# Kernel optimization log

Hardware: AMD Instinct MI355X
Metric: run time of the kernel (lower is better)

The kernel has to match this reference:

```python
import jax, jax.numpy as jnp
import numpy as np

CH = (64, 128, 256, 512)
KV = 960
H = 4          # num_attention_heads; each head owns one channel quarter
EPS = 1e-5     # InstanceNorm2d default eps
B, N = 4, 4096

def _qsplit(x):
    # (B,n,c) -> (B,H,n,c//4): contiguous quarter-split along channels (torch .split)
    b, n, c = x.shape
    return x.reshape(b, n, H, c // H).transpose(0, 2, 1, 3)

def _kvsplit(emb_all):
    # quarter j of emb_all = concat over scales of quarter j of each scale's channel block
    b, n, _ = emb_all.shape
    parts, off = [], 0
    for c in CH:
        parts.append(emb_all[:, :, off:off + c].reshape(b, n, H, c // H))
        off += c
    return jnp.concatenate(parts, axis=-1).transpose(0, 2, 1, 3)  # (B,H,n,240)

def _inorm(s):
    # InstanceNorm2d(H), affine=False: normalize each (b,h) map over its (c,k) extent
    m = jnp.mean(s, axis=(2, 3), keepdims=True)
    v = jnp.var(s, axis=(2, 3), keepdims=True)
    return (s - m) * jax.lax.rsqrt(v + EPS)

def _attend(Q, K, V):
    # Q:(B,H,n,cq)  K,V:(B,H,n,240)  -> (B,n,H*cq)  (channel attention: contract over n)
    scores = jnp.einsum('bhnc,bhnk->bhck', Q, K) / np.float32(np.sqrt(KV))
    probs = jax.nn.softmax(_inorm(scores), axis=-1)
    ctx = jnp.einsum('bhck,bhnk->bnhc', probs, V)
    b, n = ctx.shape[:2]
    return ctx.reshape(b, n, -1)

def setup_inputs() -> dict:
    key = jax.random.key(0)
    ks = iter(jax.random.split(key, 48))
    d = {}
    for name, c in [('emb1', 64), ('emb2', 128), ('emb3', 256), ('emb4', 512)]:
        d[name] = jax.random.normal(next(ks), (B, N, c), jnp.float32)
        d[name.replace('emb', 'embd')] = jax.random.normal(next(ks), (B, N, c), jnp.float32)
    d['emb_all'] = jax.random.normal(next(ks), (B, N, KV), jnp.float32)
    d['emb_alld'] = jax.random.normal(next(ks), (B, N, KV), jnp.float32)
    sc = lambda f: float(1.0 / np.sqrt(f))
    for i, c in enumerate(CH):
        c4 = c // H
        d[f'wq{i+1}'] = jax.random.uniform(next(ks), (H, c4, c4), jnp.float32, -sc(c4), sc(c4))
        d[f'wqd{i+1}'] = jax.random.uniform(next(ks), (H, c4, c4), jnp.float32, -sc(c4), sc(c4))
        d[f'wout{i+1}'] = jax.random.uniform(next(ks), (c, c), jnp.float32, -sc(c), sc(c))
        d[f'woutd{i+1}'] = jax.random.uniform(next(ks), (c, c), jnp.float32, -sc(c), sc(c))
    k4 = KV // H
    for nm in ['wk', 'wv', 'wkd', 'wvd']:  # key/value weights are shared across quarters (module uses index [0])
        d[nm] = jax.random.uniform(next(ks), (k4, k4), jnp.float32, -sc(k4), sc(k4))
    return d

def reference(emb1, emb2, emb3, emb4, emb_all, embd1, embd2, embd3, embd4, emb_alld,
              wq1, wq2, wq3, wq4, wqd1, wqd2, wqd3, wqd4,
              wk, wv, wkd, wvd,
              wout1, wout2, wout3, wout4, woutd1, woutd2, woutd3, woutd4):
    Qs = [jnp.einsum('bhnc,hdc->bhnd', _qsplit(e), w) for e, w in
          zip((emb1, emb2, emb3, emb4), (wq1, wq2, wq3, wq4))]
    Qds = [jnp.einsum('bhnc,hdc->bhnd', _qsplit(e), w) for e, w in
           zip((embd1, embd2, embd3, embd4), (wqd1, wqd2, wqd3, wqd4))]
    kvq, kvqd = _kvsplit(emb_all), _kvsplit(emb_alld)
    K  = jnp.einsum('bhnc,dc->bhnd', kvq,  wk)
    V  = jnp.einsum('bhnc,dc->bhnd', kvq,  wv)
    Kd = jnp.einsum('bhnc,dc->bhnd', kvqd, wkd)
    Vd = jnp.einsum('bhnc,dc->bhnd', kvqd, wvd)
    outs = []
    # cross-modal: optical queries attend to DSM K/V and vice versa
    for Q, w in zip(Qs, (wout1, wout2, wout3, wout4)):
        outs.append(jnp.einsum('bnc,dc->bnd', _attend(Q, Kd, Vd), w))
    for Q, w in zip(Qds, (woutd1, woutd2, woutd3, woutd4)):
        outs.append(jnp.einsum('bnc,dc->bnd', _attend(Q, K, V), w))
    return jnp.concatenate(outs, axis=-1)  # (B, N, 2*960)
```

## Files before the change

kernel.cpp:

```cpp
#include <hip/hip_runtime.h>
#include <hip/hip_bf16.h>

typedef __bf16 bf16_t;
typedef __bf16 bf16x8 __attribute__((ext_vector_type(8)));
typedef float f32x4 __attribute__((ext_vector_type(4)));

static constexpr int B_ = 4, N_ = 4096, H_ = 4;
static constexpr int KS = 40;

__device__ __forceinline__ f32x4 mfma_bf16(bf16x8 a, bf16x8 b, f32x4 c) {
  return __builtin_amdgcn_mfma_f32_16x16x32_bf16(a, b, c, 0, 0, 0);
}

__device__ __forceinline__ void stpk4(bf16_t* d, float4 v) {
  bf16_t t[4] = {(bf16_t)v.x, (bf16_t)v.y, (bf16_t)v.z, (bf16_t)v.w};
  *(uint2*)d = *(const uint2*)t;
}
__device__ __forceinline__ void stz8(bf16_t* d) { *(uint2*)d = make_uint2(0u, 0u); }

__device__ __forceinline__ int kvg(int h, int c) {
  if (c < 16)  return h * 16 + c;
  if (c < 48)  return 64 + h * 32 + c - 16;
  if (c < 112) return 192 + h * 64 + c - 48;
  return 448 + h * 128 + c - 112;
}

__device__ __forceinline__ int qsc(int r) { return (r < 16) ? 0 : (r < 48) ? 1 : (r < 112) ? 2 : 3; }

__global__ __launch_bounds__(256) void k_prep_w(
    const float* __restrict__ wk, const float* __restrict__ wv,
    const float* __restrict__ wkd, const float* __restrict__ wvd,
    const float* __restrict__ wo00, const float* __restrict__ wo01,
    const float* __restrict__ wo02, const float* __restrict__ wo03,
    const float* __restrict__ wo10, const float* __restrict__ wo11,
    const float* __restrict__ wo12, const float* __restrict__ wo13,
    bf16_t* __restrict__ Wkvb, bf16_t* __restrict__ Wob) {
  const float* wkv[4] = {wk, wv, wkd, wvd};
  const float* wo[2][4] = {{wo00, wo01, wo02, wo03}, {wo10, wo11, wo12, wo13}};
  const int soff_f4[5] = {0, 1024, 5120, 21504, 87040};
  for (int i = blockIdx.x * 256 + threadIdx.x; i < 231680; i += gridDim.x * 256) {
    if (i < 57600) {
      int t = i / 14400, r = i - t * 14400;
      float4 v = *(const float4*)(wkv[t] + r * 4);
      stpk4(Wkvb + (size_t)t * 57600 + r * 4, v);
    } else {
      int j = i - 57600;
      int mod = j / 87040, jr = j - mod * 87040;
      int s = (jr < 1024) ? 0 : (jr < 5120) ? 1 : (jr < 21504) ? 2 : 3;
      float4 v = *(const float4*)(wo[mod][s] + (jr - soff_f4[s]) * 4);
      stpk4(Wob + (size_t)mod * 348160 + jr * 4, v);
    }
  }
}

__global__ __launch_bounds__(256) void k_kvsplit(
    const float* __restrict__ eA, const float* __restrict__ eB,
    bf16_t* __restrict__ G) {
  const int TOT = 2 * 16 * 4096 * 30;
  for (int i = blockIdx.x * 256 + threadIdx.x; i < TOT; i += gridDim.x * 256) {
    int t = i / 30;
    int cg = i - t * 30;
    int mod = t >> 16;
    int row = t & 65535;
    int bh = row >> 12, n = row & 4095;
    int b = bh >> 2, h = bh & 3;
    int col = kvg(h, cg * 8);
    const float* src = (mod ? eB : eA) + ((size_t)b * N_ + n) * 960 + col;
    float4 v0 = *(const float4*)src;
    float4 v1 = *(const float4*)(src + 4);
    bf16_t o[8] = {(bf16_t)v0.x, (bf16_t)v0.y, (bf16_t)v0.z, (bf16_t)v0.w,
                   (bf16_t)v1.x, (bf16_t)v1.y, (bf16_t)v1.z, (bf16_t)v1.w};
    *(uint4*)(G + (size_t)t * 240 + cg * 8) = *(const uint4*)o;
  }
}

template <int C4>
__global__ __launch_bounds__(256) void k_proj_q(
    const float* __restrict__ e0, const float* __restrict__ w0, bf16_t* __restrict__ o0,
    const float* __restrict__ e1, const float* __restrict__ w1, bf16_t* __restrict__ o1) {
  constexpr int KP = (C4 < 32) ? 32 : C4;
  constexpr int NF = C4 / 16;
  const float* emb = blockIdx.z ? e1 : e0;
  const float* wq = blockIdx.z ? w1 : w0;
  bf16_t* qout = blockIdx.z ? o1 : o0;
  const int h = blockIdx.y;
  const int m0 = blockIdx.x * 128;
  const int b = m0 >> 12, n0 = m0 & 4095;
  const int tid = threadIdx.x, lane = tid & 63, wid = tid >> 6;
  const int l15 = lane & 15, q = lane >> 4;
  __shared__ bf16_t sA[128 * KS];
  __shared__ bf16_t sB[C4 * KS];
  const f32x4 fz = {0.f, 0.f, 0.f, 0.f};
  f32x4 acc[2][NF];
  for (int i = 0; i < 2; i++) for (int f = 0; f < NF; f++) acc[i][f] = fz;
  const float* srow = emb + ((size_t)b * N_ + n0) * (H_ * C4) + h * C4;
  const float* wb = wq + h * C4 * C4;
  for (int k0 = 0; k0 < KP; k0 += 32) {
    __syncthreads();
    for (int idx = tid; idx < 1024; idx += 256) {
      int r = idx >> 3, cg = idx & 7, c = k0 + cg * 4;
      if (c < C4) stpk4(&sA[r * KS + cg * 4], *(const float4*)(srow + (size_t)r * (H_ * C4) + c));
      else stz8(&sA[r * KS + cg * 4]);
    }
    for (int idx = tid; idx < C4 * 8; idx += 256) {
      int dd = idx >> 3, cg = idx & 7, c = k0 + cg * 4;
      if (c < C4) stpk4(&sB[dd * KS + cg * 4], *(const float4*)(wb + dd * C4 + c));
      else stz8(&sB[dd * KS + cg * 4]);
    }
    __syncthreads();
    const bf16_t* ap = &sA[(wid * 32 + l15) * KS + q * 8];
    bf16x8 a0 = *(const bf16x8*)ap;
    bf16x8 a1 = *(const bf16x8*)(ap + 16 * KS);
    for (int f = 0; f < NF; f++) {
      bf16x8 bb = *(const bf16x8*)&sB[(16 * f + l15) * KS + q * 8];
      acc[0][f] = mfma_bf16(a0, bb, acc[0][f]);
      acc[1][f] = mfma_bf16(a1, bb, acc[1][f]);
    }
  }
  bf16_t* qbh = qout + (size_t)(b * H_ + h) * C4 * 4096;
  for (int i = 0; i < 2; i++)
    for (int f = 0; f < NF; f++) {
      bf16_t pk[4];
      for (int r = 0; r < 4; r++) pk[r] = (bf16_t)acc[i][f][r];
      *(uint2*)(qbh + (size_t)(16 * f + l15) * 4096 + n0 + wid * 32 + 16 * i + q * 4) =
          *(const uint2*)pk;
    }
}

__global__ __launch_bounds__(512) void k_proj_kv(
    const bf16_t* __restrict__ G, const bf16_t* __restrict__ Wkvb,
    bf16_t* __restrict__ Kt0, bf16_t* __restrict__ V0,
    bf16_t* __restrict__ Kt1, bf16_t* __restrict__ V1) {
  const int mod = blockIdx.y;
  const bf16_t* src = G + (size_t)mod * ((size_t)B_ * H_ * N_ * 240);
  const bf16_t* wK = Wkvb + (size_t)(2 * mod) * 57600;
  const bf16_t* wV = Wkvb + (size_t)(2 * mod + 1) * 57600;
  bf16_t* Kt = mod ? Kt1 : Kt0;
  bf16_t* V = mod ? V1 : V0;
  const int m0 = blockIdx.x * 128;
  const int bh = m0 >> 12, n0 = m0 & 4095;
  const int tid = threadIdx.x, lane = tid & 63, wid = tid >> 6;
  const int l15 = lane & 15, q = lane >> 4;
  __shared__ bf16_t sA[128 * KS];
  __shared__ bf16_t sB[2][240 * KS];
  const f32x4 fz = {0.f, 0.f, 0.f, 0.f};
  f32x4 accK[15], accV[15];
  for (int f = 0; f < 15; f++) { accK[f] = fz; accV[f] = fz; }
  const bf16_t* arow = src + (size_t)m0 * 240;
  const uint4 z4 = make_uint4(0u, 0u, 0u, 0u);

  const int ar = tid >> 2, ag = tid & 3;
  int bm[4], bd[4], bg[4];
#pragma unroll
  for (int j = 0; j < 4; j++) {
    int idx = tid + 512 * j;
    bm[j] = idx >= 960;
    int jj = idx - (bm[j] ? 960 : 0);
    bd[j] = jj >> 2; bg[j] = jj & 3;
  }
  uint4 ra, rb0, rb1, rb2, rb3;

#define KV_LOAD(K0)                                                                    \
  {                                                                                    \
    int c = (K0) + ag * 8;                                                             \
    ra = (c < 240) ? *(const uint4*)(arow + (size_t)ar * 240 + c) : z4;                \
    int c0_ = (K0) + bg[0] * 8;                                                        \
    rb0 = (c0_ < 240) ? *(const uint4*)((bm[0] ? wV : wK) + bd[0] * 240 + c0_) : z4;   \
    int c1_ = (K0) + bg[1] * 8;                                                        \
    rb1 = (c1_ < 240) ? *(const uint4*)((bm[1] ? wV : wK) + bd[1] * 240 + c1_) : z4;   \
    int c2_ = (K0) + bg[2] * 8;                                                        \
    rb2 = (c2_ < 240) ? *(const uint4*)((bm[2] ? wV : wK) + bd[2] * 240 + c2_) : z4;   \
    if (tid < 384) {                                                                   \
      int c3_ = (K0) + bg[3] * 8;                                                      \
      rb3 = (c3_ < 240) ? *(const uint4*)((bm[3] ? wV : wK) + bd[3] * 240 + c3_) : z4; \
    }                                                                                  \
  }
#define KV_WRITE()                                                                     \
  {                                                                                    \
    *(uint4*)&sA[ar * KS + ag * 8] = ra;                                               \
    *(uint4*)&sB[bm[0]][bd[0] * KS + bg[0] * 8] = rb0;                                 \
    *(uint4*)&sB[bm[1]][bd[1] * KS + bg[1] * 8] = rb1;                                 \
    *(uint4*)&sB[bm[2]][bd[2] * KS + bg[2] * 8] = rb2;                                 \
    if (tid < 384) *(uint4*)&sB[bm[3]][bd[3] * KS + bg[3] * 8] = rb3;                  \
  }

  KV_LOAD(0);
  KV_WRITE();
  for (int t = 0; t < 8; t++) {
    if (t < 7) KV_LOAD((t + 1) * 32);
    __syncthreads();
    bf16x8 a = *(const bf16x8*)&sA[(wid * 16 + l15) * KS + q * 8];
#pragma unroll
    for (int f = 0; f < 15; f++) {
      bf16x8 bk = *(const bf16x8*)&sB[0][(16 * f + l15) * KS + q * 8];
      bf16x8 bv = *(const bf16x8*)&sB[1][(16 * f + l15) * KS + q * 8];
      accK[f] = mfma_bf16(a, bk, accK[f]);
      accV[f] = mfma_bf16(a, bv, accV[f]);
    }
    __syncthreads();
    if (t < 7) KV_WRITE();
  }
#undef KV_LOAD
#undef KV_WRITE

  for (int f = 0; f < 15; f++) {
    bf16_t pk[4];
    for (int r = 0; r < 4; r++) pk[r] = (bf16_t)accK[f][r];
    bf16_t* dst = Kt + ((size_t)bh * 240 + 16 * f + l15) * 4096 + n0 + wid * 16 + q * 4;
    *(uint2*)dst = *(const uint2*)pk;
  }
  bf16_t* orow = V + ((size_t)bh * N_ + n0) * 240;
  for (int f = 0; f < 15; f++)
    for (int r = 0; r < 4; r++) {
      int mm = wid * 16 + q * 4 + r;
      orow[(size_t)mm * 240 + 16 * f + l15] = (bf16_t)accV[f][r];
    }
}

__global__ __launch_bounds__(512) void k_scores_all(
    const bf16_t* __restrict__ Qb, const bf16_t* __restrict__ Kt0,
    const bf16_t* __restrict__ Kt1, float* __restrict__ probs) {
  const size_t KV1 = (size_t)B_ * H_ * N_ * 240;
  const size_t PB1 = (size_t)B_ * H_ * 240 * 240;
  const int qcum[4] = {0, 16, 48, 112};
  const int bh = blockIdx.x;
  const int mod = blockIdx.y >> 3, chunk = blockIdx.y & 7;
  const int ch0 = chunk * 512;
  const bf16_t* ktp = mod ? Kt0 : Kt1;
  const int tid = threadIdx.x, lane = tid & 63, wid = tid >> 6;
  const int l15 = lane & 15, q = lane >> 4;
  __shared__ bf16_t sQ[240 * KS];
  __shared__ bf16_t sK[240 * KS];
  const f32x4 fz = {0.f, 0.f, 0.f, 0.f};
  f32x4 acc[2][15];
  for (int i = 0; i < 2; i++) for (int f = 0; f < 15; f++) acc[i][f] = fz;

  const int row0 = tid >> 2, g8 = (tid & 3) * 8;
  const int row1v = row0 + 128;
  const int row1 = (row1v < 240) ? row1v : 239;
  const bool hasR1 = (tid < 448);
  int s0i = qsc(row0), s1i = qsc(row1);
  const bf16_t* qp0 = Qb + (size_t)mod * KV1 + (size_t)65536 * qcum[s0i] +
                      ((size_t)bh * (16 << s0i) + (row0 - qcum[s0i])) * 4096 + ch0 + g8;
  const bf16_t* qp1 = Qb + (size_t)mod * KV1 + (size_t)65536 * qcum[s1i] +
                      ((size_t)bh * (16 << s1i) + (row1 - qcum[s1i])) * 4096 + ch0 + g8;
  const bf16_t* kp0 = ktp + ((size_t)bh * 240 + row0) * 4096 + ch0 + g8;
  const bf16_t* kp1 = ktp + ((size_t)bh * 240 + row1) * 4096 + ch0 + g8;
  uint4 rq0, rq1, rk0, rk1;

#define SC_LOAD(K0)                                   \
  {                                                   \
    rq0 = *(const uint4*)(qp0 + (K0));                \
    rk0 = *(const uint4*)(kp0 + (K0));                \
    if (hasR1) {                                      \
      rq1 = *(const uint4*)(qp1 + (K0));              \
      rk1 = *(const uint4*)(kp1 + (K0));              \
    }                                                 \
  }
#define SC_WRITE()                                    \
  {                                                   \
    *(uint4*)&sQ[row0 * KS + g8] = rq0;               \
    *(uint4*)&sK[row0 * KS + g8] = rk0;               \
    if (hasR1) {                                      \
      *(uint4*)&sQ[row1v * KS + g8] = rq1;            \
      *(uint4*)&sK[row1v * KS + g8] = rk1;            \
    }                                                 \
  }

  const int cf0 = wid, cf1 = wid + 8;
  SC_LOAD(0);
  SC_WRITE();
  for (int t = 0; t < 16; t++) {
    if (t < 15) SC_LOAD((t + 1) * 32);
    __syncthreads();
    bf16x8 af0 = *(const bf16x8*)&sQ[(16 * cf0 + l15) * KS + q * 8];
    bf16x8 af1;
    if (cf1 < 15) af1 = *(const bf16x8*)&sQ[(16 * cf1 + l15) * KS + q * 8];
#pragma unroll
    for (int f = 0; f < 15; f++) {
      bf16x8 bb = *(const bf16x8*)&sK[(16 * f + l15) * KS + q * 8];
      acc[0][f] = mfma_bf16(af0, bb, acc[0][f]);
      if (cf1 < 15) acc[1][f] = mfma_bf16(af1, bb, acc[1][f]);
    }
    __syncthreads();
    if (t < 15) SC_WRITE();
  }
#undef SC_LOAD
#undef SC_WRITE

  const float rs = 0.0322748612183951f;
  for (int ci = 0; ci < 2; ci++) {
    int cf = wid + 8 * ci;
    if (cf >= 15) continue;
    int cbase = 16 * cf;
    int s = qsc(cbase);
    float* pb = probs + (size_t)mod * PB1 +
                ((size_t)16 * qcum[s] + (size_t)bh * (16 << s)) * 240;
    int crow = cbase - qcum[s] + q * 4;
    for (int f = 0; f < 15; f++)
      for (int r = 0; r < 4; r++)
        atomicAdd(&pb[(size_t)(crow + r) * 240 + 16 * f + l15], acc[ci][f][r] * rs);
  }
}

__global__ __launch_bounds__(256) void k_inorm_softmax(float* __restrict__ p0,
                                                       float* __restrict__ p1, int c4) {
  float* p = (blockIdx.z ? p1 : p0) + (size_t)blockIdx.x * c4 * 240;
  const int tid = threadIdx.x;
  const int tot = c4 * 240;
  float s = 0.f, s2 = 0.f;
  for (int idx = tid; idx < tot; idx += 256) {
    float v = p[idx];
    s += v; s2 += v * v;
  }
#pragma unroll
  for (int off = 32; off > 0; off >>= 1) {
    s += __shfl_xor(s, off);
    s2 += __shfl_xor(s2, off);
  }
  __shared__ float rsum[4], rsum2[4], smv[2];
  const int wid = tid >> 6, lane = tid & 63;
  if (lane == 0) { rsum[wid] = s; rsum2[wid] = s2; }
  __syncthreads();
  if (tid == 0) {
    float ts = rsum[0] + rsum[1] + rsum[2] + rsum[3];
    float ts2 = rsum2[0] + rsum2[1] + rsum2[2] + rsum2[3];
    float mean = ts / tot;
    float var = ts2 / tot - mean * mean;
    smv[0] = mean; smv[1] = rsqrtf(var + 1e-5f);
  }
  __syncthreads();
  const float mean = smv[0], rstd = smv[1];
  for (int c = wid; c < c4; c += 4) {
    float* row = p + (size_t)c * 240;
    float x[4]; float mx = -1e30f;
#pragma unroll
    for (int t = 0; t < 4; t++) {
      int k = lane + 64 * t;
      x[t] = (k < 240) ? (row[k] - mean) * rstd : -1e30f;
      mx = fmaxf(mx, x[t]);
    }
#pragma unroll
    for (int off = 32; off > 0; off >>= 1) mx = fmaxf(mx, __shfl_xor(mx, off));
    float e[4], sum = 0.f;
#pragma unroll
    for (int t = 0; t < 4; t++) {
      int k = lane + 64 * t;
      e[t] = (k < 240) ? expf(x[t] - mx) : 0.f;
      sum += e[t];
    }
#pragma unroll
    for (int off = 32; off > 0; off >>= 1) sum += __shfl_xor(sum, off);
    const float inv = 1.f / sum;
#pragma unroll
    for (int t = 0; t < 4; t++) {
      int k = lane + 64 * t;
      if (k < 240) row[k] = e[t] * inv;
    }
  }
}

__global__ __launch_bounds__(512) void k_pv_all(
    const float* __restrict__ probs, const bf16_t* __restrict__ V0,
    const bf16_t* __restrict__ V1, bf16_t* __restrict__ ctx0, bf16_t* __restrict__ ctx1) {
  const size_t PB1 = (size_t)B_ * H_ * 240 * 240;
  const int qcum[4] = {0, 16, 48, 112};
  const int chof[4] = {0, 64, 192, 448};
  const int bh = blockIdx.y, b = bh >> 2, h = bh & 3;
  const int mod = blockIdx.z;
  const int n0 = blockIdx.x * 128;
  const bf16_t* v = mod ? V0 : V1;
  bf16_t* ctx = mod ? ctx1 : ctx0;
  const float* pb_all = probs + (size_t)mod * PB1;
  const int tid = threadIdx.x, lane = tid & 63, wid = tid >> 6;
  const int l15 = lane & 15, q = lane >> 4;
  __shared__ bf16_t sV[128 * KS];
  __shared__ bf16_t sP[240 * KS];
  const f32x4 fz = {0.f, 0.f, 0.f, 0.f};
  f32x4 acc[15];
  for (int f = 0; f < 15; f++) acc[f] = fz;
  const bf16_t* vrow = v + ((size_t)bh * N_ + n0) * 240;
  for (int k0 = 0; k0 < 256; k0 += 32) {
    __syncthreads();
    {
      int r = tid >> 2, g = tid & 3, k = k0 + g * 8;
      if (k < 240) *(uint4*)&sV[r * KS + g * 8] = *(const uint4*)(vrow + (size_t)r * 240 + k);
      else *(uint4*)&sV[r * KS + g * 8] = make_uint4(0u, 0u, 0u, 0u);
    }
    for (int idx = tid; idx < 1920; idx += 512) {
      int cc = idx >> 3, cg = idx & 7, k = k0 + cg * 4;
      if (k < 240) {
        int s = qsc(cc);
        const float* prow = pb_all +
            ((size_t)16 * qcum[s] + (size_t)bh * (16 << s) + (cc - qcum[s])) * 240;
        stpk4(&sP[cc * KS + cg * 4], *(const float4*)(prow + k));
      } else {
        stz8(&sP[cc * KS + cg * 4]);
      }
    }
    __syncthreads();
    bf16x8 a = *(const bf16x8*)&sV[(wid * 16 + l15) * KS + q * 8];
#pragma unroll
    for (int f = 0; f < 15; f++) {
      bf16x8 bb = *(const bf16x8*)&sP[(16 * f + l15) * KS + q * 8];
      acc[f] = mfma_bf16(a, bb, acc[f]);
    }
  }
  for (int f = 0; f < 15; f++) {
    int s = qsc(16 * f);
    int colbase = chof[s] + h * (16 << s) + 16 * f - qcum[s];
    for (int r = 0; r < 4; r++) {
      int mm = 16 * wid + q * 4 + r;
      ctx[((size_t)b * N_ + n0 + mm) * 960 + colbase + l15] = (bf16_t)acc[f][r];
    }
  }
}

template <int CS>
__global__ __launch_bounds__(256) void k_wout(
    const bf16_t* __restrict__ c0p, const bf16_t* __restrict__ w0, int ob0,
    const bf16_t* __restrict__ c1p, const bf16_t* __restrict__ w1, int ob1,
    float* __restrict__ out, int chof) {
  constexpr int DT = (CS < 128) ? CS : 128;
  constexpr int NF = DT / 16;
  constexpr int DB = CS / DT;
  const int mod = blockIdx.z / DB, dch = blockIdx.z % DB;
  const bf16_t* ctx = mod ? c1p : c0p;
  const bf16_t* w = mod ? w1 : w0;
  const int obase = (mod ? ob1 : ob0) + dch * DT;
  const int m0 = blockIdx.x * 128;
  const int b = m0 >> 12, n0 = m0 & 4095;
  const int tid = threadIdx.x, lane = tid & 63, wid = tid >> 6;
  const int l15 = lane & 15, q = lane >> 4;
  __shared__ bf16_t sA[128 * KS];
  __shared__ bf16_t sB[DT * KS];
  const f32x4 fz = {0.f, 0.f, 0.f, 0.f};
  f32x4 acc[2][NF];
  for (int i = 0; i < 2; i++) for (int f = 0; f < NF; f++) acc[i][f] = fz;
  const bf16_t* arow = ctx + ((size_t)b * N_ + n0) * 960 + chof;
  const bf16_t* wb = w + (size_t)dch * DT * CS;
  for (int k0 = 0; k0 < CS; k0 += 32) {
    __syncthreads();
    for (int idx = tid; idx < 512; idx += 256) {
      int r = idx >> 2, g = idx & 3, k = k0 + g * 8;
      *(uint4*)&sA[r * KS + g * 8] = *(const uint4*)(arow + (size_t)r * 960 + k);
    }
    for (int idx = tid; idx < DT * 4; idx += 256) {
      int dd = idx >> 2, g = idx & 3, k = k0 + g * 8;
      *(uint4*)&sB[dd * KS + g * 8] = *(const uint4*)(wb + (size_t)dd * CS + k);
    }
    __syncthreads();
    const bf16_t* ap = &sA[(wid * 32 + l15) * KS + q * 8];
    bf16x8 a0 = *(const bf16x8*)ap;
    bf16x8 a1 = *(const bf16x8*)(ap + 16 * KS);
    for (int f = 0; f < NF; f++) {
      bf16x8 bb = *(const bf16x8*)&sB[(16 * f + l15) * KS + q * 8];
      acc[0][f] = mfma_bf16(a0, bb, acc[0][f]);
      acc[1][f] = mfma_bf16(a1, bb, acc[1][f]);
    }
  }
  float* orow = out + ((size_t)b * N_ + n0) * 1920 + obase;
  for (int i = 0; i < 2; i++)
    for (int f = 0; f < NF; f++)
      for (int r = 0; r < 4; r++) {
        int mm = wid * 32 + 16 * i + q * 4 + r;
        orow[(size_t)mm * 1920 + 16 * f + l15] = acc[i][f][r];
      }
}

extern "C" void kernel_launch(void* const* d_in, const int* in_sizes, int n_in,
                              void* d_out, int out_size, void* d_ws, size_t ws_size,
                              hipStream_t stream) {
  (void)in_sizes; (void)n_in; (void)out_size; (void)ws_size;
  const float* emb[2][4];
  const float* wq[2][4];
  const float* wo[2][4];
  for (int s = 0; s < 4; s++) {
    emb[0][s] = (const float*)d_in[2 * s];
    emb[1][s] = (const float*)d_in[2 * s + 1];
    wq[0][s] = (const float*)d_in[10 + 4 * s];
    wq[1][s] = (const float*)d_in[11 + 4 * s];
    wo[0][s] = (const float*)d_in[12 + 4 * s];
    wo[1][s] = (const float*)d_in[13 + 4 * s];
  }
  const float* emb_all = (const float*)d_in[8];
  const float* emb_alld = (const float*)d_in[9];
  const float* wkp = (const float*)d_in[26];
  const float* wvp = (const float*)d_in[27];
  const float* wkdp = (const float*)d_in[28];
  const float* wvdp = (const float*)d_in[29];
  float* out = (float*)d_out;

  bf16_t* w16 = (bf16_t*)d_ws;
  const size_t KV1 = (size_t)B_ * H_ * N_ * 240;
  const size_t PB1 = (size_t)B_ * H_ * 240 * 240;
  bf16_t* Kt0 = w16;
  bf16_t* Kt1 = w16 + KV1;
  bf16_t* V0 = w16 + 2 * KV1;
  bf16_t* V1 = w16 + 3 * KV1;
  bf16_t* Qb = w16 + 4 * KV1;
  float* probs = (float*)(w16 + 6 * KV1);
  bf16_t* Wkvb = (bf16_t*)(probs + 2 * PB1);
  bf16_t* Wob = Wkvb + 230400;
  const int qcum[4] = {0, 16, 48, 112};
  const int chof[4] = {0, 64, 192, 448};
  const int soff[4] = {0, 4096, 20480, 86016};
  const dim3 blk(256);

  k_prep_w<<<dim3(256), blk, 0, stream>>>(wkp, wvp, wkdp, wvdp,
      wo[0][0], wo[0][1], wo[0][2], wo[0][3], wo[1][0], wo[1][1], wo[1][2], wo[1][3],
      Wkvb, Wob);
  hipMemsetAsync(probs, 0, 2 * PB1 * sizeof(float), stream);

  k_kvsplit<<<dim3(2048), blk, 0, stream>>>(emb_all, emb_alld, Qb);
  k_proj_kv<<<dim3(B_ * H_ * N_ / 128, 2), dim3(512), 0, stream>>>(
      Qb, Wkvb, Kt0, V0, Kt1, V1);
  for (int s = 0; s < 4; s++) {
    bf16_t* q0 = Qb + (size_t)B_ * H_ * N_ * qcum[s];
    bf16_t* q1 = q0 + KV1;
    dim3 g(B_ * N_ / 128, H_, 2);
    switch (s) {
      case 0: k_proj_q<16><<<g, blk, 0, stream>>>(emb[0][s], wq[0][s], q0, emb[1][s], wq[1][s], q1); break;
      case 1: k_proj_q<32><<<g, blk, 0, stream>>>(emb[0][s], wq[0][s], q0, emb[1][s], wq[1][s], q1); break;
      case 2: k_proj_q<64><<<g, blk, 0, stream>>>(emb[0][s], wq[0][s], q0, emb[1][s], wq[1][s], q1); break;
      case 3: k_proj_q<128><<<g, blk, 0, stream>>>(emb[0][s], wq[0][s], q0, emb[1][s], wq[1][s], q1); break;
    }
  }
  k_scores_all<<<dim3(B_ * H_, 16), dim3(512), 0, stream>>>(Qb, Kt0, Kt1, probs);
  for (int s = 0; s < 4; s++) {
    float* p0 = probs + (size_t)B_ * H_ * qcum[s] * 240;
    float* p1 = p0 + PB1;
    k_inorm_softmax<<<dim3(B_ * H_, 1, 2), blk, 0, stream>>>(p0, p1, 16 << s);
  }
  k_pv_all<<<dim3(N_ / 128, B_ * H_, 2), dim3(512), 0, stream>>>(
      probs, V0, V1, Qb, Qb + KV1);
  for (int s = 0; s < 4; s++) {
    const bf16_t* cx0 = Qb;
    const bf16_t* cx1 = Qb + KV1;
    const bf16_t* w0 = Wob + soff[s];
    const bf16_t* w1 = Wob + 348160 + soff[s];
    const int cs = 64 << s;
    const int db = (cs < 128) ? 1 : cs / 128;
    dim3 g(B_ * N_ / 128, 1, 2 * db);
    switch (s) {
      case 0: k_wout<64><<<g, blk, 0, stream>>>(cx0, w0, chof[s], cx1, w1, 960 + chof[s], out, chof[s]); break;
      case 1: k_wout<128><<<g, blk, 0, stream>>>(cx0, w0, chof[s], cx1, w1, 960 + chof[s], out, chof[s]); break;
      case 2: k_wout<256><<<g, blk, 0, stream>>>(cx0, w0, chof[s], cx1, w1, 960 + chof[s], out, chof[s]); break;
      case 3: k_wout<512><<<g, blk, 0, stream>>>(cx0, w0, chof[s], cx1, w1, 960 + chof[s], out, chof[s]); break;
    }
  }
}
```

Before: 826.6 us.

## Fold V projection into probs and apply attention to raw KV split

Uses associativity: instead of projecting V = G·Wv^T for every token, the softmax probabilities (240x240 per batch-head) are multiplied by the V weight in a small new kernel, and the PV kernel then consumes the raw split KV input directly. The projection kernel now computes only K for both modalities in one launch, sharing the loop structure. This removes a large GEMM and its V writeback at the cost of one tiny fp32 matmul on probs and a slight change in rounding order.

```diff
diff --git a/kernel.cpp b/kernel.cpp
--- a/kernel.cpp
+++ b/kernel.cpp
@@ -127,26 +127,23 @@
     }
 }
 
-__global__ __launch_bounds__(512) void k_proj_kv(
+__global__ __launch_bounds__(512) void k_proj_k2(
     const bf16_t* __restrict__ G, const bf16_t* __restrict__ Wkvb,
-    bf16_t* __restrict__ Kt0, bf16_t* __restrict__ V0,
-    bf16_t* __restrict__ Kt1, bf16_t* __restrict__ V1) {
-  const int mod = blockIdx.y;
-  const bf16_t* src = G + (size_t)mod * ((size_t)B_ * H_ * N_ * 240);
-  const bf16_t* wK = Wkvb + (size_t)(2 * mod) * 57600;
-  const bf16_t* wV = Wkvb + (size_t)(2 * mod + 1) * 57600;
-  bf16_t* Kt = mod ? Kt1 : Kt0;
-  bf16_t* V = mod ? V1 : V0;
+    bf16_t* __restrict__ Kt0, bf16_t* __restrict__ Kt1) {
+  const size_t KV1 = (size_t)B_ * H_ * N_ * 240;
+  const bf16_t* wK0 = Wkvb;
+  const bf16_t* wK1 = Wkvb + 2 * 57600;
   const int m0 = blockIdx.x * 128;
   const int bh = m0 >> 12, n0 = m0 & 4095;
   const int tid = threadIdx.x, lane = tid & 63, wid = tid >> 6;
   const int l15 = lane & 15, q = lane >> 4;
-  __shared__ bf16_t sA[128 * KS];
+  __shared__ bf16_t sA[2][128 * KS];
   __shared__ bf16_t sB[2][240 * KS];
   const f32x4 fz = {0.f, 0.f, 0.f, 0.f};
-  f32x4 accK[15], accV[15];
-  for (int f = 0; f < 15; f++) { accK[f] = fz; accV[f] = fz; }
-  const bf16_t* arow = src + (size_t)m0 * 240;
+  f32x4 acc[2][15];
+  for (int m = 0; m < 2; m++) for (int f = 0; f < 15; f++) acc[m][f] = fz;
+  const bf16_t* arow0 = G + (size_t)m0 * 240;
+  const bf16_t* arow1 = G + KV1 + (size_t)m0 * 240;
   const uint4 z4 = make_uint4(0u, 0u, 0u, 0u);
 
   const int ar = tid >> 2, ag = tid & 3;
@@ -158,63 +155,63 @@
     int jj = idx - (bm[j] ? 960 : 0);
     bd[j] = jj >> 2; bg[j] = jj & 3;
   }
-  uint4 ra, rb0, rb1, rb2, rb3;
-
-#define KV_LOAD(K0)                                                                    \
-  {                                                                                    \
-    int c = (K0) + ag * 8;                                                             \
-    ra = (c < 240) ? *(const uint4*)(arow + (size_t)ar * 240 + c) : z4;                \
-    int c0_ = (K0) + bg[0] * 8;                                                        \
-    rb0 = (c0_ < 240) ? *(const uint4*)((bm[0] ? wV : wK) + bd[0] * 240 + c0_) : z4;   \
-    int c1_ = (K0) + bg[1] * 8;                                                        \
-    rb1 = (c1_ < 240) ? *(const uint4*)((bm[1] ? wV : wK) + bd[1] * 240 + c1_) : z4;   \
-    int c2_ = (K0) + bg[2] * 8;                                                        \
-    rb2 = (c2_ < 240) ? *(const uint4*)((bm[2] ? wV : wK) + bd[2] * 240 + c2_) : z4;   \
-    if (tid < 384) {                                                                   \
-      int c3_ = (K0) + bg[3] * 8;                                                      \
-      rb3 = (c3_ < 240) ? *(const uint4*)((bm[3] ? wV : wK) + bd[3] * 240 + c3_) : z4; \
-    }                                                                                  \
-  }
-#define KV_WRITE()                                                                     \
-  {                                                                                    \
-    *(uint4*)&sA[ar * KS + ag * 8] = ra;                                               \
-    *(uint4*)&sB[bm[0]][bd[0] * KS + bg[0] * 8] = rb0;                                 \
-    *(uint4*)&sB[bm[1]][bd[1] * KS + bg[1] * 8] = rb1;                                 \
-    *(uint4*)&sB[bm[2]][bd[2] * KS + bg[2] * 8] = rb2;                                 \
-    if (tid < 384) *(uint4*)&sB[bm[3]][bd[3] * KS + bg[3] * 8] = rb3;                  \
-  }
-
-  KV_LOAD(0);
-  KV_WRITE();
+  uint4 ra0, ra1, rb0, rb1, rb2, rb3;
+
+#define K2_LOAD(K0)                                                                     \
+  {                                                                                     \
+    int ca = (K0) + ag * 8;                                                             \
+    ra0 = (ca < 240) ? *(const uint4*)(arow0 + (size_t)ar * 240 + ca) : z4;             \
+    ra1 = (ca < 240) ? *(const uint4*)(arow1 + (size_t)ar * 240 + ca) : z4;             \
+    int c0_ = (K0) + bg[0] * 8;                                                         \
+    rb0 = (c0_ < 240) ? *(const uint4*)((bm[0] ? wK1 : wK0) + bd[0] * 240 + c0_) : z4;  \
+    int c1_ = (K0) + bg[1] * 8;                                                         \
+    rb1 = (c1_ < 240) ? *(const uint4*)((bm[1] ? wK1 : wK0) + bd[1] * 240 + c1_) : z4;  \
+    int c2_ = (K0) + bg[2] * 8;                                                         \
+    rb2 = (c2_ < 240) ? *(const uint4*)((bm[2] ? wK1 : wK0) + bd[2] * 240 + c2_) : z4;  \
+    if (tid < 384) {                                                                    \
+      int c3_ = (K0) + bg[3] * 8;                                                       \
+      rb3 = (c3_ < 240) ? *(const uint4*)((bm[3] ? wK1 : wK0) + bd[3] * 240 + c3_) : z4;\
+    }                                                                                   \
+  }
+#define K2_WRITE()                                                                      \
+  {                                                                                     \
+    *(uint4*)&sA[0][ar * KS + ag * 8] = ra0;                                            \
+    *(uint4*)&sA[1][ar * KS + ag * 8] = ra1;                                            \
+    *(uint4*)&sB[bm[0]][bd[0] * KS + bg[0] * 8] = rb0;                                  \
+    *(uint4*)&sB[bm[1]][bd[1] * KS + bg[1] * 8] = rb1;                                  \
+    *(uint4*)&sB[bm[2]][bd[2] * KS + bg[2] * 8] = rb2;                                  \
+    if (tid < 384) *(uint4*)&sB[bm[3]][bd[3] * KS + bg[3] * 8] = rb3;                   \
+  }
+
+  K2_LOAD(0);
+  K2_WRITE();
   for (int t = 0; t < 8; t++) {
-    if (t < 7) KV_LOAD((t + 1) * 32);
-    __syncthreads();
-    bf16x8 a = *(const bf16x8*)&sA[(wid * 16 + l15) * KS + q * 8];
+    if (t < 7) K2_LOAD((t + 1) * 32);
+    __syncthreads();
+    bf16x8 a0 = *(const bf16x8*)&sA[0][(wid * 16 + l15) * KS + q * 8];
+    bf16x8 a1 = *(const bf16x8*)&sA[1][(wid * 16 + l15) * KS + q * 8];
 #pragma unroll
     for (int f = 0; f < 15; f++) {
-      bf16x8 bk = *(const bf16x8*)&sB[0][(16 * f + l15) * KS + q * 8];
-      bf16x8 bv = *(const bf16x8*)&sB[1][(16 * f + l15) * KS + q * 8];
-      accK[f] = mfma_bf16(a, bk, accK[f]);
-      accV[f] = mfma_bf16(a, bv, accV[f]);
-    }
-    __syncthreads();
-    if (t < 7) KV_WRITE();
-  }
-#undef KV_LOAD
-#undef KV_WRITE
-
-  for (int f = 0; f < 15; f++) {
-    bf16_t pk[4];
-    for (int r = 0; r < 4; r++) pk[r] = (bf16_t)accK[f][r];
-    bf16_t* dst = Kt + ((size_t)bh * 240 + 16 * f + l15) * 4096 + n0 + wid * 16 + q * 4;
-    *(uint2*)dst = *(const uint2*)pk;
-  }
-  bf16_t* orow = V + ((size_t)bh * N_ + n0) * 240;
-  for (int f = 0; f < 15; f++)
-    for (int r = 0; r < 4; r++) {
-      int mm = wid * 16 + q * 4 + r;
-      orow[(size_t)mm * 240 + 16 * f + l15] = (bf16_t)accV[f][r];
-    }
+      bf16x8 b0 = *(const bf16x8*)&sB[0][(16 * f + l15) * KS + q * 8];
+      bf16x8 b1 = *(const bf16x8*)&sB[1][(16 * f + l15) * KS + q * 8];
+      acc[0][f] = mfma_bf16(a0, b0, acc[0][f]);
+      acc[1][f] = mfma_bf16(a1, b1, acc[1][f]);
+    }
+    __syncthreads();
+    if (t < 7) K2_WRITE();
+  }
+#undef K2_LOAD
+#undef K2_WRITE
+
+  for (int m = 0; m < 2; m++) {
+    bf16_t* Kt = m ? Kt1 : Kt0;
+    for (int f = 0; f < 15; f++) {
+      bf16_t pk[4];
+      for (int r = 0; r < 4; r++) pk[r] = (bf16_t)acc[m][f][r];
+      bf16_t* dst = Kt + ((size_t)bh * 240 + 16 * f + l15) * 4096 + n0 + wid * 16 + q * 4;
+      *(uint2*)dst = *(const uint2*)pk;
+    }
+  }
 }
 
 __global__ __launch_bounds__(512) void k_scores_all(
@@ -357,6 +354,37 @@
       int k = lane + 64 * t;
       if (k < 240) row[k] = e[t] * inv;
     }
+  }
+}
+
+__global__ __launch_bounds__(256) void k_pwv(
+    float* __restrict__ probs, const float* __restrict__ wv,
+    const float* __restrict__ wvd) {
+  const size_t PB1 = (size_t)B_ * H_ * 240 * 240;
+  const int mod = blockIdx.y;
+  const float* w = mod ? wv : wvd;
+  float* rows = probs + (size_t)mod * PB1 + (size_t)blockIdx.x * 16 * 240;
+  const int tid = threadIdx.x;
+  __shared__ float sP[16][241];
+  __shared__ float sW[240][16];
+  for (int idx = tid; idx < 960; idx += 256) {
+    int r = idx / 60, g = idx - r * 60;
+    float4 v = *(const float4*)(rows + (size_t)r * 240 + g * 4);
+    sP[r][g * 4 + 0] = v.x; sP[r][g * 4 + 1] = v.y;
+    sP[r][g * 4 + 2] = v.z; sP[r][g * 4 + 3] = v.w;
+  }
+  const int c = tid >> 4, j = tid & 15;
+  for (int jc = 0; jc < 15; jc++) {
+    __syncthreads();
+    for (int idx = tid; idx < 960; idx += 256) {
+      int k = idx >> 2, g = idx & 3;
+      *(float4*)&sW[k][g * 4] = *(const float4*)(w + (size_t)k * 240 + jc * 16 + g * 4);
+    }
+    __syncthreads();
+    float acc = 0.f;
+#pragma unroll 8
+    for (int k = 0; k < 240; k++) acc += sP[c][k] * sW[k][j];
+    rows[(size_t)c * 240 + jc * 16 + j] = acc;
   }
 }
 
@@ -496,8 +524,8 @@
   const size_t PB1 = (size_t)B_ * H_ * 240 * 240;
   bf16_t* Kt0 = w16;
   bf16_t* Kt1 = w16 + KV1;
-  bf16_t* V0 = w16 + 2 * KV1;
-  bf16_t* V1 = w16 + 3 * KV1;
+  bf16_t* G0 = w16 + 2 * KV1;
+  bf16_t* G1 = G0 + KV1;
   bf16_t* Qb = w16 + 4 * KV1;
   float* probs = (float*)(w16 + 6 * KV1);
   bf16_t* Wkvb = (bf16_t*)(probs + 2 * PB1);
@@ -512,9 +540,8 @@
       Wkvb, Wob);
   hipMemsetAsync(probs, 0, 2 * PB1 * sizeof(float), stream);
 
-  k_kvsplit<<<dim3(2048), blk, 0, stream>>>(emb_all, emb_alld, Qb);
-  k_proj_kv<<<dim3(B_ * H_ * N_ / 128, 2), dim3(512), 0, stream>>>(
-      Qb, Wkvb, Kt0, V0, Kt1, V1);
+  k_kvsplit<<<dim3(2048), blk, 0, stream>>>(emb_all, emb_alld, G0);
+  k_proj_k2<<<dim3(B_ * H_ * N_ / 128), dim3(512), 0, stream>>>(G0, Wkvb, Kt0, Kt1);
   for (int s = 0; s < 4; s++) {
     bf16_t* q0 = Qb + (size_t)B_ * H_ * N_ * qcum[s];
     bf16_t* q1 = q0 + KV1;
@@ -532,8 +559,9 @@
     float* p1 = p0 + PB1;
     k_inorm_softmax<<<dim3(B_ * H_, 1, 2), blk, 0, stream>>>(p0, p1, 16 << s);
   }
+  k_pwv<<<dim3(240, 2), blk, 0, stream>>>(probs, wvp, wvdp);
   k_pv_all<<<dim3(N_ / 128, B_ * H_, 2), dim3(512), 0, stream>>>(
-      probs, V0, V1, Qb, Qb + KV1);
+      probs, G0, G1, Qb, Qb + KV1);
   for (int s = 0; s < 4; s++) {
     const bf16_t* cx0 = Qb;
     const bf16_t* cx1 = Qb + KV1;
```

Result: slower. 865.9 us (+4.8%).
